# Performance work log

Measured on AMD Instinct MI355X. Metric: run time of the kernel, lower is better.

Reference implementation:

```python
import jax, jax.numpy as jnp
import numpy as np

NUM_HEADS = 8
DIM = 256
NW = 64  # number of windows per batch element


def setup_inputs() -> dict:
    key = jax.random.key(0)
    k_x, k_m, k_ws, k_wm, k_wp, k_bp = jax.random.split(key, 6)
    B_, N, C = 512, 128, DIM
    x = jax.random.normal(k_x, (B_, N, C), dtype=jnp.float32)
    # 0 / -100 additive attention mask (stand-in for the 0/-inf shift-window mask)
    mask = jnp.where(jax.random.uniform(k_m, (NW, N, N)) < 0.5, 0.0, -100.0).astype(jnp.float32)
    std = 0.02
    w_qkv_self = jax.random.normal(k_ws, (3 * C, C), dtype=jnp.float32) * std
    w_qkv_mut = jax.random.normal(k_wm, (3 * C, C), dtype=jnp.float32) * std
    w_proj = jax.random.normal(k_wp, (C, 2 * C), dtype=jnp.float32) * std
    b_proj = jax.random.normal(k_bp, (C,), dtype=jnp.float32) * std
    return {"x": x, "mask": mask, "w_qkv_self": w_qkv_self,
            "w_qkv_mut": w_qkv_mut, "w_proj": w_proj, "b_proj": b_proj}


def _split_qkv(x, w):
    # x: (B_, N, C); w: (3C, C) torch Linear weight -> y = x @ w.T
    B_, N, C = x.shape
    d = C // NUM_HEADS
    qkv = (x @ w.T).reshape(B_, N, 3, NUM_HEADS, d).transpose(2, 0, 3, 1, 4)
    return qkv[0], qkv[1], qkv[2]  # each (B_, H, N, d)


def _attention(q, k, v, mask, scale):
    # q,k,v: (B_, H, n, d); mask: (nW, Nfull, Nfull) additive
    B_, H, n, d = q.shape
    nW = mask.shape[0]
    attn = jnp.einsum('bhnd,bhmd->bhnm', q * scale, k)  # (B_, H, n, n)
    attn = attn.reshape(B_ // nW, nW, H, n, n) + mask[None, :, None, :n, :n]
    attn = jax.nn.softmax(attn.reshape(B_, H, n, n), axis=-1)
    out = jnp.einsum('bhnm,bhmd->bhnd', attn, v)
    return out.transpose(0, 2, 1, 3).reshape(B_, n, H * d)  # (B_, n, C)


def reference(x, mask, w_qkv_self, w_qkv_mut, w_proj, b_proj):
    B_, N, C = x.shape
    scale = (C // NUM_HEADS) ** (-0.5)
    # self window attention
    q, k, v = _split_qkv(x, w_qkv_self)
    x_out = _attention(q, k, v, mask, scale)  # (B_, N, C)
    # mutual (cross-frame) attention between the two halves of the window
    qm, km, vm = _split_qkv(x, w_qkv_mut)
    h = N // 2
    q1, q2 = qm[:, :, :h], qm[:, :, h:]
    k1, k2 = km[:, :, :h], km[:, :, h:]
    v1, v2 = vm[:, :, :h], vm[:, :, h:]
    x1_aligned = _attention(q2, k1, v1, mask, scale)  # (B_, N//2, C)
    x2_aligned = _attention(q1, k2, v2, mask, scale)  # (B_, N//2, C)
    x_mut = jnp.concatenate([x1_aligned, x2_aligned], axis=1)  # (B_, N, C)
    x_cat = jnp.concatenate([x_mut, x_out], axis=2)  # (B_, N, 2C)
    return x_cat @ w_proj.T + b_proj  # (B_, N, C)
```

## Files before the change

kernel.cpp:

```cpp
#include <hip/hip_runtime.h>
#include <stdint.h>

typedef __bf16 bf16x4 __attribute__((ext_vector_type(4)));
typedef __bf16 bf16x8 __attribute__((ext_vector_type(8)));
typedef float f32x4 __attribute__((ext_vector_type(4)));

#define DEVI __device__ __forceinline__

DEVI ushort bfbits(float f) {
  union { __bf16 b; ushort u; } v;
  v.b = (__bf16)f;
  return v.u;
}

DEVI void gload16(const void* g, void* l) {
  auto* gp = reinterpret_cast<const __attribute__((address_space(1))) uint32_t*>(
      reinterpret_cast<uintptr_t>(g));
  auto* lp = reinterpret_cast<__attribute__((address_space(3))) uint32_t*>(
      reinterpret_cast<uintptr_t>(l));
  __builtin_amdgcn_global_load_lds(gp, lp, 16, 0, 0);
}

__global__ __launch_bounds__(256) void cvt_x(const float* __restrict__ in,
                                             ushort* __restrict__ out) {
  int i = (blockIdx.x * 256 + threadIdx.x) * 4;
  float4 v = *(const float4*)(in + i);
  ushort4 o;
  o.x = bfbits(v.x); o.y = bfbits(v.y); o.z = bfbits(v.z); o.w = bfbits(v.w);
  *(ushort4*)(out + i) = o;
}

__global__ __launch_bounds__(256) void cvt_w(const float* __restrict__ ws,
                                             const float* __restrict__ wm,
                                             const float* __restrict__ wp,
                                             ushort* __restrict__ wqkv,
                                             ushort* __restrict__ wproj) {
  int i = blockIdx.x * 256 + threadIdx.x;
  if (i < 196608)       wqkv[i] = bfbits(ws[i]);
  else if (i < 393216)  wqkv[i] = bfbits(wm[i - 196608]);
  else                  wproj[i - 393216] = bfbits(wp[i - 393216]);
}

template <int KF, int NH>
DEVI void attn_body(const ushort* Qs, const ushort* Ks, const ushort* Vt,
                    ushort* Ps, const float* mrow, ushort* ob,
                    int qrow0, int kvbase, int orow0, int mrow0,
                    int lr, int lc) {
  const float L2E = 1.4426950408889634f;

  f32x4 sacc[2][KF];
#pragma unroll
  for (int mf = 0; mf < 2; ++mf)
#pragma unroll
    for (int nf = 0; nf < KF; ++nf) sacc[mf][nf] = (f32x4){0.f, 0.f, 0.f, 0.f};

  bf16x8 aq[2];
#pragma unroll
  for (int mf = 0; mf < 2; ++mf) {
    int r = qrow0 + mf * 16 + lr;
    aq[mf] = *(const bf16x8*)(Qs + r * 32 + ((lc ^ ((r >> 1) & 3)) * 8));
  }
  __builtin_amdgcn_s_setprio(1);
#pragma unroll
  for (int nf = 0; nf < KF; ++nf) {
    int r = kvbase + nf * 16 + lr;
    bf16x8 bk = *(const bf16x8*)(Ks + r * 32 + ((lc ^ ((r >> 1) & 3)) * 8));
#pragma unroll
    for (int mf = 0; mf < 2; ++mf)
      sacc[mf][nf] = __builtin_amdgcn_mfma_f32_16x16x32_bf16(aq[mf], bk, sacc[mf][nf], 0, 0, 0);
  }
  __builtin_amdgcn_s_setprio(0);

#pragma unroll
  for (int mf = 0; mf < 2; ++mf)
#pragma unroll
    for (int nf = 0; nf < KF; ++nf)
#pragma unroll
      for (int r = 0; r < 4; ++r) {
        int row = mrow0 + mf * 16 + lc * 4 + r;
        int col = nf * 16 + lr;
        sacc[mf][nf][r] = fmaf(mrow[row * 128 + col], L2E, sacc[mf][nf][r]);
      }
  float sinv[2][4];
#pragma unroll
  for (int mf = 0; mf < 2; ++mf)
#pragma unroll
    for (int r = 0; r < 4; ++r) {
      float s = 0.f;
#pragma unroll
      for (int nf = 0; nf < KF; ++nf) {
        float e = __builtin_amdgcn_exp2f(sacc[mf][nf][r]);
        sacc[mf][nf][r] = e;
        s += e;
      }
#pragma unroll
      for (int d = 1; d < 16; d <<= 1) s += __shfl_xor(s, d);
      sinv[mf][r] = __builtin_amdgcn_rcpf(s);
    }

  __syncthreads();

  f32x4 oacc[2][2];
#pragma unroll
  for (int mf = 0; mf < 2; ++mf)
#pragma unroll
    for (int nf = 0; nf < 2; ++nf) oacc[mf][nf] = (f32x4){0.f, 0.f, 0.f, 0.f};

#pragma unroll
  for (int hf = 0; hf < NH; ++hf) {
#pragma unroll
    for (int mf = 0; mf < 2; ++mf)
#pragma unroll
      for (int r = 0; r < 4; ++r) {
        int prow = orow0 + mf * 16 + lc * 4 + r;
#pragma unroll
        for (int nf2 = 0; nf2 < 4; ++nf2) {
          int col = nf2 * 16 + lr;
          int grp = (col >> 3) ^ (prow & 7);
          Ps[prow * 64 + grp * 8 + (col & 7)] = bfbits(sacc[mf][hf * 4 + nf2][r]);
        }
      }
    __builtin_amdgcn_s_setprio(1);
#pragma unroll
    for (int ks = 0; ks < 2; ++ks) {
      bf16x8 pf[2], vf[2];
#pragma unroll
      for (int mf = 0; mf < 2; ++mf) {
        int prow = orow0 + mf * 16 + lr;
        int grp = (ks * 4 + lc) ^ (prow & 7);
        pf[mf] = *(const bf16x8*)(Ps + prow * 64 + grp * 8);
      }
#pragma unroll
      for (int nf = 0; nf < 2; ++nf)
        vf[nf] = *(const bf16x8*)(Vt + (nf * 16 + lr) * 136 + kvbase + hf * 64 + ks * 32 + lc * 8);
#pragma unroll
      for (int mf = 0; mf < 2; ++mf)
#pragma unroll
        for (int nf = 0; nf < 2; ++nf)
          oacc[mf][nf] = __builtin_amdgcn_mfma_f32_16x16x32_bf16(pf[mf], vf[nf], oacc[mf][nf], 0, 0, 0);
    }
    __builtin_amdgcn_s_setprio(0);
  }

#pragma unroll
  for (int mf = 0; mf < 2; ++mf)
#pragma unroll
    for (int nf = 0; nf < 2; ++nf)
#pragma unroll
      for (int r = 0; r < 4; ++r) {
        int row = orow0 + mf * 16 + lc * 4 + r;
        int col = nf * 16 + lr;
        ob[(size_t)row * 512 + col] = bfbits(oacc[mf][nf][r] * sinv[mf][r]);
      }
}

__global__ __launch_bounds__(256) void attn_fused(const ushort* __restrict__ xb,
                                                  const ushort* __restrict__ wqkv,
                                                  const float* __restrict__ mask,
                                                  ushort* __restrict__ xcat) {
  __shared__ __align__(16) uint8_t smem[28672];
  ushort* xs0 = (ushort*)smem;
  ushort* wl0 = (ushort*)(smem + 8192);
  ushort* xs1 = (ushort*)(smem + 14336);
  ushort* wl1 = (ushort*)(smem + 22528);
  ushort* Qs  = (ushort*)smem;
  ushort* Ks  = (ushort*)(smem + 8192);
  ushort* Vt  = (ushort*)(smem + 16384);
  ushort* Ps  = (ushort*)smem;

  const int bid = blockIdx.x;
  const int c = bid & 7;
  const int u = bid >> 3;
  const int m = u & 1;
  const int h = (u >> 1) & 7;
  const int b = (u >> 4) * 8 + c;
  const int wmask = b & 63;
  const int t = threadIdx.x;
  const int wid = t >> 6, l = t & 63;
  const int lr = l & 15, lc = l >> 4;
  const float qscale = 0.17677669529663687f * 1.4426950408889634f;

  const ushort* xrow = xb + (size_t)b * 128 * 256;
  const int wbase = m * 768;

  auto STAGE = [&](int kk, ushort* xs, ushort* wl) {
#pragma unroll
    for (int p = 0; p < 2; ++p) {
      int slot = t + p * 256;
      int row = slot >> 2, cs = slot & 3;
      int cd = cs ^ ((row >> 1) & 3);
      gload16(xrow + (size_t)row * 256 + kk + cd * 8, xs + slot * 8);
    }
    {
      int slot = t;
      int row = slot >> 2, cs = slot & 3;
      int cd = cs ^ ((row >> 1) & 3);
      int grow = wbase + (row >> 5) * 256 + h * 32 + (row & 31);
      gload16(wqkv + (size_t)grow * 256 + kk + cd * 8, wl + slot * 8);
    }
    if (t < 128) {
      int slot = t + 256;
      int row = slot >> 2, cs = slot & 3;
      int cd = cs ^ ((row >> 1) & 3);
      int grow = wbase + (row >> 5) * 256 + h * 32 + (row & 31);
      gload16(wqkv + (size_t)grow * 256 + kk + cd * 8, wl + slot * 8);
    }
  };

  f32x4 pacc[2][6];
#pragma unroll
  for (int mf = 0; mf < 2; ++mf)
#pragma unroll
    for (int n = 0; n < 6; ++n) pacc[mf][n] = (f32x4){0.f, 0.f, 0.f, 0.f};

  STAGE(0, xs0, wl0);
#pragma unroll
  for (int k = 0; k < 8; ++k) {
    __syncthreads();
    if (k < 7) {
      if ((k & 1) == 0) STAGE((k + 1) * 32, xs1, wl1);
      else              STAGE((k + 1) * 32, xs0, wl0);
    }
    const ushort* xs = (k & 1) ? xs1 : xs0;
    const ushort* wl = (k & 1) ? wl1 : wl0;

    bf16x8 ax[2];
#pragma unroll
    for (int mf = 0; mf < 2; ++mf) {
      int r = wid * 32 + mf * 16 + lr;
      ax[mf] = *(const bf16x8*)(xs + r * 32 + ((lc ^ ((r >> 1) & 3)) * 8));
    }
    __builtin_amdgcn_s_setprio(1);
#pragma unroll
    for (int n = 0; n < 6; ++n) {
      int r = n * 16 + lr;
      bf16x8 bw = *(const bf16x8*)(wl + r * 32 + ((lc ^ ((r >> 1) & 3)) * 8));
#pragma unroll
      for (int mf = 0; mf < 2; ++mf)
        pacc[mf][n] = __builtin_amdgcn_mfma_f32_16x16x32_bf16(ax[mf], bw, pacc[mf][n], 0, 0, 0);
    }
    __builtin_amdgcn_s_setprio(0);
  }
  __syncthreads();

#pragma unroll
  for (int mf = 0; mf < 2; ++mf) {
#pragma unroll
    for (int n = 0; n < 4; ++n)
#pragma unroll
      for (int j = 0; j < 4; ++j) {
        int row = wid * 32 + mf * 16 + lc * 4 + j;
        int d = (n & 1) * 16 + lr;
        float v = pacc[mf][n][j];
        if (n < 2) v *= qscale;
        int sw = ((d >> 3) ^ ((row >> 1) & 3)) * 8 + (d & 7);
        (n < 2 ? Qs : Ks)[row * 32 + sw] = bfbits(v);
      }
#pragma unroll
    for (int k = 0; k < 2; ++k) {
      bf16x4 pk;
#pragma unroll
      for (int j = 0; j < 4; ++j) pk[j] = (__bf16)pacc[mf][4 + k][j];
      int d = k * 16 + lr;
      int row0 = wid * 32 + mf * 16 + lc * 4;
      *(bf16x4*)(Vt + d * 136 + row0) = pk;
    }
  }
  __syncthreads();

  const float* mrow = mask + (size_t)wmask * 16384;

  if (m == 0) {
    ushort* ob = xcat + (size_t)b * 128 * 512 + 256 + h * 32;
    attn_body<8, 2>(Qs, Ks, Vt, Ps, mrow, ob,
                    wid * 32, 0,
                    wid * 32, wid * 32, lr, lc);
  } else {
    const int half = wid >> 1, sub = wid & 1;
    ushort* ob = xcat + (size_t)b * 128 * 512 + h * 32;
    attn_body<4, 1>(Qs, Ks, Vt, Ps, mrow, ob,
                    (half ? 0 : 64) + sub * 32, half ? 64 : 0,
                    half * 64 + sub * 32, sub * 32, lr, lc);
  }
}

__global__ __launch_bounds__(256) void gemm_proj(const ushort* __restrict__ A,
                                                 const ushort* __restrict__ B,
                                                 const float* __restrict__ bias,
                                                 float* __restrict__ out) {
  __shared__ ushort As[64 * 32];
  __shared__ ushort Bs[256 * 32];
  const int t = threadIdx.x, tm = blockIdx.x;
  const int w = t >> 6, l = t & 63;
  const int wc = w * 64;
  const int lr = l & 15, lc = l >> 4;
  const ushort* Ab = A + (size_t)tm * 64 * 512;

  f32x4 acc[4][4];
#pragma unroll
  for (int m = 0; m < 4; ++m)
#pragma unroll
    for (int n = 0; n < 4; ++n) acc[m][n] = (f32x4){0.f, 0.f, 0.f, 0.f};

  for (int kk = 0; kk < 512; kk += 32) {
    __syncthreads();
    {
      int slot = t;
      int row = slot >> 2, cs = slot & 3;
      int cd = cs ^ ((row >> 1) & 3);
      gload16(Ab + (size_t)row * 512 + kk + cd * 8, As + slot * 8);
    }
#pragma unroll
    for (int p = 0; p < 4; ++p) {
      int slot = t + p * 256;
      int row = slot >> 2, cs = slot & 3;
      int cd = cs ^ ((row >> 1) & 3);
      gload16(B + (size_t)row * 512 + kk + cd * 8, Bs + slot * 8);
    }
    __syncthreads();

    bf16x8 af[4], bfr[4];
#pragma unroll
    for (int m = 0; m < 4; ++m) {
      int r = m * 16 + lr;
      af[m] = *(const bf16x8*)(As + r * 32 + ((lc ^ ((r >> 1) & 3)) * 8));
    }
#pragma unroll
    for (int n = 0; n < 4; ++n) {
      int r = wc + n * 16 + lr;
      bfr[n] = *(const bf16x8*)(Bs + r * 32 + ((lc ^ ((r >> 1) & 3)) * 8));
    }
    __builtin_amdgcn_s_setprio(1);
#pragma unroll
    for (int m = 0; m < 4; ++m)
#pragma unroll
      for (int n = 0; n < 4; ++n)
        acc[m][n] = __builtin_amdgcn_mfma_f32_16x16x32_bf16(af[m], bfr[n], acc[m][n], 0, 0, 0);
    __builtin_amdgcn_s_setprio(0);
  }

#pragma unroll
  for (int m = 0; m < 4; ++m)
#pragma unroll
    for (int n = 0; n < 4; ++n)
#pragma unroll
      for (int r = 0; r < 4; ++r) {
        int row = tm * 64 + m * 16 + lc * 4 + r;
        int col = wc + n * 16 + lr;
        out[(size_t)row * 256 + col] = acc[m][n][r] + bias[col];
      }
}

extern "C" void kernel_launch(void* const* d_in, const int* in_sizes, int n_in,
                              void* d_out, int out_size, void* d_ws, size_t ws_size,
                              hipStream_t stream) {
  const float* x = (const float*)d_in[0];
  const float* mask = (const float*)d_in[1];
  const float* w_qkv_self = (const float*)d_in[2];
  const float* w_qkv_mut = (const float*)d_in[3];
  const float* w_proj = (const float*)d_in[4];
  const float* b_proj = (const float*)d_in[5];
  float* out = (float*)d_out;

  uint8_t* ws = (uint8_t*)d_ws;
  ushort* xb    = (ushort*)(ws);
  ushort* wqkv  = (ushort*)(ws + 33554432);
  ushort* wproj = (ushort*)(ws + 34340864);
  ushort* xcat  = (ushort*)d_out;

  cvt_x<<<dim3(16384), dim3(256), 0, stream>>>(x, xb);
  cvt_w<<<dim3(2048), dim3(256), 0, stream>>>(w_qkv_self, w_qkv_mut, w_proj, wqkv, wproj);
  attn_fused<<<dim3(8192), dim3(256), 0, stream>>>(xb, wqkv, mask, xcat);
  gemm_proj<<<dim3(1024), dim3(256), 0, stream>>>(xcat, wproj, b_proj, out);
}
```

Before: 178.3 us.

## Fuse self and mutual attention into one block per batch-head

Each block now handles both the self and the mutual QKV projection for one (batch, head) pair, instead of launching separate blocks per branch. The x tile is staged into LDS once and multiplied against 12 weight fragments, which halves the redundant x reads and halves the grid size. In exchange, LDS grows to about 50KB and the accumulator registers double, which can lower occupancy. The two attention bodies also now run back to back in the same block, which serializes work that previously ran in separate blocks.

```diff
diff --git a/kernel.cpp b/kernel.cpp
--- a/kernel.cpp
+++ b/kernel.cpp
@@ -158,22 +158,24 @@
                                                   const ushort* __restrict__ wqkv,
                                                   const float* __restrict__ mask,
                                                   ushort* __restrict__ xcat) {
-  __shared__ __align__(16) uint8_t smem[28672];
+  __shared__ __align__(16) uint8_t smem[50176];
   ushort* xs0 = (ushort*)smem;
   ushort* wl0 = (ushort*)(smem + 8192);
-  ushort* xs1 = (ushort*)(smem + 14336);
-  ushort* wl1 = (ushort*)(smem + 22528);
-  ushort* Qs  = (ushort*)smem;
-  ushort* Ks  = (ushort*)(smem + 8192);
-  ushort* Vt  = (ushort*)(smem + 16384);
+  ushort* xs1 = (ushort*)(smem + 20480);
+  ushort* wl1 = (ushort*)(smem + 28672);
+  ushort* sQs = (ushort*)smem;
+  ushort* sKs = (ushort*)(smem + 8192);
+  ushort* sVt = (ushort*)(smem + 16384);
+  ushort* mQs = (ushort*)(smem + 25088);
+  ushort* mKs = (ushort*)(smem + 33280);
+  ushort* mVt = (ushort*)(smem + 41472);
   ushort* Ps  = (ushort*)smem;
 
   const int bid = blockIdx.x;
   const int c = bid & 7;
   const int u = bid >> 3;
-  const int m = u & 1;
-  const int h = (u >> 1) & 7;
-  const int b = (u >> 4) * 8 + c;
+  const int h = u & 7;
+  const int b = (u >> 3) * 8 + c;
   const int wmask = b & 63;
   const int t = threadIdx.x;
   const int wid = t >> 6, l = t & 63;
@@ -181,7 +183,6 @@
   const float qscale = 0.17677669529663687f * 1.4426950408889634f;
 
   const ushort* xrow = xb + (size_t)b * 128 * 256;
-  const int wbase = m * 768;
 
   auto STAGE = [&](int kk, ushort* xs, ushort* wl) {
 #pragma unroll
@@ -191,27 +192,21 @@
       int cd = cs ^ ((row >> 1) & 3);
       gload16(xrow + (size_t)row * 256 + kk + cd * 8, xs + slot * 8);
     }
-    {
-      int slot = t;
+#pragma unroll
+    for (int p = 0; p < 3; ++p) {
+      int slot = t + p * 256;
       int row = slot >> 2, cs = slot & 3;
       int cd = cs ^ ((row >> 1) & 3);
-      int grow = wbase + (row >> 5) * 256 + h * 32 + (row & 31);
+      int grow = (row >> 5) * 256 + h * 32 + (row & 31);
       gload16(wqkv + (size_t)grow * 256 + kk + cd * 8, wl + slot * 8);
     }
-    if (t < 128) {
-      int slot = t + 256;
-      int row = slot >> 2, cs = slot & 3;
-      int cd = cs ^ ((row >> 1) & 3);
-      int grow = wbase + (row >> 5) * 256 + h * 32 + (row & 31);
-      gload16(wqkv + (size_t)grow * 256 + kk + cd * 8, wl + slot * 8);
-    }
   };
 
-  f32x4 pacc[2][6];
-#pragma unroll
-  for (int mf = 0; mf < 2; ++mf)
-#pragma unroll
-    for (int n = 0; n < 6; ++n) pacc[mf][n] = (f32x4){0.f, 0.f, 0.f, 0.f};
+  f32x4 pacc[2][12];
+#pragma unroll
+  for (int mf = 0; mf < 2; ++mf)
+#pragma unroll
+    for (int n = 0; n < 12; ++n) pacc[mf][n] = (f32x4){0.f, 0.f, 0.f, 0.f};
 
   STAGE(0, xs0, wl0);
 #pragma unroll
@@ -232,7 +227,7 @@
     }
     __builtin_amdgcn_s_setprio(1);
 #pragma unroll
-    for (int n = 0; n < 6; ++n) {
+    for (int n = 0; n < 12; ++n) {
       int r = n * 16 + lr;
       bf16x8 bw = *(const bf16x8*)(wl + r * 32 + ((lc ^ ((r >> 1) & 3)) * 8));
 #pragma unroll
@@ -244,41 +239,48 @@
   __syncthreads();
 
 #pragma unroll
-  for (int mf = 0; mf < 2; ++mf) {
-#pragma unroll
-    for (int n = 0; n < 4; ++n)
-#pragma unroll
-      for (int j = 0; j < 4; ++j) {
-        int row = wid * 32 + mf * 16 + lc * 4 + j;
-        int d = (n & 1) * 16 + lr;
-        float v = pacc[mf][n][j];
-        if (n < 2) v *= qscale;
-        int sw = ((d >> 3) ^ ((row >> 1) & 3)) * 8 + (d & 7);
-        (n < 2 ? Qs : Ks)[row * 32 + sw] = bfbits(v);
-      }
-#pragma unroll
-    for (int k = 0; k < 2; ++k) {
-      bf16x4 pk;
-#pragma unroll
-      for (int j = 0; j < 4; ++j) pk[j] = (__bf16)pacc[mf][4 + k][j];
-      int d = k * 16 + lr;
-      int row0 = wid * 32 + mf * 16 + lc * 4;
-      *(bf16x4*)(Vt + d * 136 + row0) = pk;
+  for (int g = 0; g < 2; ++g) {
+    ushort* Qg = g ? mQs : sQs;
+    ushort* Kg = g ? mKs : sKs;
+    ushort* Vg = g ? mVt : sVt;
+#pragma unroll
+    for (int mf = 0; mf < 2; ++mf) {
+#pragma unroll
+      for (int nn = 0; nn < 4; ++nn)
+#pragma unroll
+        for (int j = 0; j < 4; ++j) {
+          int row = wid * 32 + mf * 16 + lc * 4 + j;
+          int d = (nn & 1) * 16 + lr;
+          float v = pacc[mf][g * 6 + nn][j];
+          if (nn < 2) v *= qscale;
+          int sw = ((d >> 3) ^ ((row >> 1) & 3)) * 8 + (d & 7);
+          (nn < 2 ? Qg : Kg)[row * 32 + sw] = bfbits(v);
+        }
+#pragma unroll
+      for (int k = 0; k < 2; ++k) {
+        bf16x4 pk;
+#pragma unroll
+        for (int j = 0; j < 4; ++j) pk[j] = (__bf16)pacc[mf][g * 6 + 4 + k][j];
+        int d = k * 16 + lr;
+        int row0 = wid * 32 + mf * 16 + lc * 4;
+        *(bf16x4*)(Vg + d * 136 + row0) = pk;
+      }
     }
   }
   __syncthreads();
 
   const float* mrow = mask + (size_t)wmask * 16384;
 
-  if (m == 0) {
+  {
     ushort* ob = xcat + (size_t)b * 128 * 512 + 256 + h * 32;
-    attn_body<8, 2>(Qs, Ks, Vt, Ps, mrow, ob,
+    attn_body<8, 2>(sQs, sKs, sVt, Ps, mrow, ob,
                     wid * 32, 0,
                     wid * 32, wid * 32, lr, lc);
-  } else {
+  }
+  {
     const int half = wid >> 1, sub = wid & 1;
     ushort* ob = xcat + (size_t)b * 128 * 512 + h * 32;
-    attn_body<4, 1>(Qs, Ks, Vt, Ps, mrow, ob,
+    attn_body<4, 1>(mQs, mKs, mVt, Ps, mrow, ob,
                     (half ? 0 : 64) + sub * 32, half ? 64 : 0,
                     half * 64 + sub * 32, sub * 32, lr, lc);
   }
@@ -370,6 +372,6 @@
 
   cvt_x<<<dim3(16384), dim3(256), 0, stream>>>(x, xb);
   cvt_w<<<dim3(2048), dim3(256), 0, stream>>>(w_qkv_self, w_qkv_mut, w_proj, wqkv, wproj);
-  attn_fused<<<dim3(8192), dim3(256), 0, stream>>>(xb, wqkv, mask, xcat);
+  attn_fused<<<dim3(4096), dim3(256), 0, stream>>>(xb, wqkv, mask, xcat);
   gemm_proj<<<dim3(1024), dim3(256), 0, stream>>>(xcat, wproj, b_proj, out);
 }
```

Measured after the change: 220.9 us. +23.9%, slower.
